# Kernel optimization log

Measured on AMD Instinct MI355X. Metric: run time of the kernel, lower is better.

Reference implementation:

```python
import jax, jax.numpy as jnp
import numpy as np

D_MODEL = 1024
D_STATE = 16
D_CONV = 4
EXPAND = 2
D_INNER = D_MODEL * EXPAND


def setup_inputs() -> dict:
    key = jax.random.key(0)
    ks = jax.random.split(key, 8)
    B, L = 2, 2048
    x = jax.random.normal(ks[0], (B, L, D_MODEL), dtype=jnp.float32)
    # in_proj: Linear(d_model -> 2*d_inner), no bias
    W_in = jax.random.normal(ks[1], (D_MODEL, 2 * D_INNER), dtype=jnp.float32) / np.sqrt(D_MODEL)
    # depthwise conv1d: (d_inner, 1, d_conv) + bias
    conv_w = jax.random.normal(ks[2], (D_INNER, 1, D_CONV), dtype=jnp.float32) / np.sqrt(D_CONV)
    conv_b = jax.random.normal(ks[3], (D_INNER,), dtype=jnp.float32) * 0.01
    # x_proj: Linear(d_inner -> 2*d_state + 1), no bias
    W_x = jax.random.normal(ks[4], (D_INNER, 2 * D_STATE + 1), dtype=jnp.float32) / np.sqrt(D_INNER)
    # A_log ~ Uniform(-log(d_state), -1)
    A_log = jax.random.uniform(ks[5], (D_INNER, D_STATE), dtype=jnp.float32,
                               minval=-np.log(D_STATE), maxval=-1.0)
    D_param = jnp.ones((D_INNER,), dtype=jnp.float32)
    W_out = jax.random.normal(ks[6], (D_INNER, D_MODEL), dtype=jnp.float32) / np.sqrt(D_INNER)
    return {"x": x, "W_in": W_in, "conv_w": conv_w, "conv_b": conv_b,
            "W_x": W_x, "A_log": A_log, "D_param": D_param, "W_out": W_out}


def _selective_scan(x, delta, A, Bm, Cm):
    # x:(B,L,D), delta:(B,L), A:(D,N), Bm/Cm:(B,L,N)
    Bsz, L, Dd = x.shape
    N = A.shape[1]
    h0 = jnp.zeros((Bsz, Dd, N), dtype=x.dtype)

    def step(h, inp):
        dt, Bt, Ct, xt = inp  # (B,), wait dt:(B,), Bt:(B,N), Ct:(B,N), xt:(B,D)
        A_bar = jnp.exp(dt[:, None, None] * A)          # (B,D,N)
        dB = (dt[:, None] * Bt)[:, None, :]             # (B,1,N)
        h = A_bar * h + dB * xt[:, :, None]             # (B,D,N)
        y = jnp.einsum('bn,bdn->bd', Ct, h)             # (B,D)
        return h, y

    xs = (jnp.swapaxes(delta, 0, 1), jnp.swapaxes(Bm, 0, 1),
          jnp.swapaxes(Cm, 0, 1), jnp.swapaxes(x, 0, 1))
    _, ys = jax.lax.scan(step, h0, xs)                  # ys: (L,B,D)
    return jnp.swapaxes(ys, 0, 1)


def reference(x, W_in, conv_w, conv_b, W_x, A_log, D_param, W_out):
    B, L, _ = x.shape
    xr = x @ W_in                                       # (B,L,2*Di)
    x_inner, res = jnp.split(xr, 2, axis=-1)
    # causal depthwise conv: left-pad d_conv-1, valid conv == torch slice [:L]
    xc = jnp.swapaxes(x_inner, 1, 2)                    # (B,Di,L)
    xc = jax.lax.conv_general_dilated(
        xc, conv_w, window_strides=(1,), padding=[(D_CONV - 1, 0)],
        dimension_numbers=('NCH', 'OIH', 'NCH'), feature_group_count=D_INNER)
    xc = xc + conv_b[None, :, None]
    xc = jnp.swapaxes(xc, 1, 2)                         # (B,L,Di)
    xc = jax.nn.silu(xc)
    ssm_params = xc @ W_x                               # (B,L,1+2N)
    delta = jax.nn.softplus(ssm_params[..., 0])         # (B,L)
    Bm = ssm_params[..., 1:1 + D_STATE]                 # (B,L,N)
    Cm = ssm_params[..., 1 + D_STATE:]                  # (B,L,N)
    A = -jnp.exp(A_log)                                 # (Di,N)
    y = _selective_scan(xc, delta, A, Bm, Cm)           # (B,L,Di)
    y = y + xc * D_param[None, None, :]
    y = y * jax.nn.silu(res)
    return y @ W_out                                    # (B,L,d_model)
```

## Files before the change

kernel.cpp:

```cpp
#include <hip/hip_runtime.h>

#define L_SEQ 2048
#define NB    2
#define DMOD  1024
#define DIN   2048
#define NST   16
#define NROWS (NB*L_SEQ)
#define CL    64
#define NC    (L_SEQ/CL)

typedef unsigned short u16;
typedef _Float16 half8 __attribute__((ext_vector_type(8)));
typedef float f32x4 __attribute__((ext_vector_type(4)));
typedef short short8 __attribute__((ext_vector_type(8)));

__device__ __forceinline__ float siluf(float v){ return v / (1.f + __expf(-v)); }
__device__ __forceinline__ u16 f2h_bits(float v){ _Float16 h = (_Float16)v; return __builtin_bit_cast(u16, h); }
__device__ __forceinline__ float h2f(u16 v){ return (float)__builtin_bit_cast(_Float16, v); }
__device__ __forceinline__ float fexp2(float x){
#if __has_builtin(__builtin_amdgcn_exp2f)
    return __builtin_amdgcn_exp2f(x);
#else
    return __expf(x * 0.69314718056f);
#endif
}

__device__ __forceinline__ void gload16(const u16* g, u16* l)
{
    __builtin_amdgcn_global_load_lds(
        (const __attribute__((address_space(1))) void*)g,
        (__attribute__((address_space(3))) void*)l,
        16, 0, 0);
}

#define BARRIER() do { asm volatile("" ::: "memory"); __builtin_amdgcn_s_barrier(); asm volatile("" ::: "memory"); } while (0)
#define VMCNT0()  asm volatile("s_waitcnt vmcnt(0)" ::: "memory")
#define VMCNT2()  asm volatile("s_waitcnt vmcnt(2)" ::: "memory")
#define VMCNT4()  asm volatile("s_waitcnt vmcnt(4)" ::: "memory")
#define VMCNT8()  asm volatile("s_waitcnt vmcnt(8)" ::: "memory")

__global__ __launch_bounds__(256)
void prep_inputs(const float* __restrict__ x, const float* __restrict__ W_in,
                 const float* __restrict__ W_out, const float* __restrict__ Wx,
                 u16* __restrict__ x16, u16* __restrict__ Bt1,
                 u16* __restrict__ Bt3, u16* __restrict__ WxT16)
{
    __shared__ float s[64][65];
    const int bid = blockIdx.x, tid = threadIdx.x;
    if (bid < 4096) {
        int i = bid * 256 + tid;
        float4 v = ((const float4*)x)[i];
        ushort4 o;
        o.x = f2h_bits(v.x); o.y = f2h_bits(v.y); o.z = f2h_bits(v.z); o.w = f2h_bits(v.w);
        *(ushort4*)&x16[(size_t)i * 4] = o;
    } else if (bid < 5632) {
        const float* in; u16* outT; int R, C, rblk, cblk;
        if (bid < 5120) { int b = bid - 4096; in = W_in;  outT = Bt1; R = 1024; C = 4096; cblk = b & 63; rblk = b >> 6; }
        else            { int b = bid - 5120; in = W_out; outT = Bt3; R = 2048; C = 1024; cblk = b & 15; rblk = b >> 4; }
        int r0 = rblk * 64, c0 = cblk * 64;
        int tc = tid & 63, ty = tid >> 6;
        #pragma unroll
        for (int j = 0; j < 16; j++) {
            int r = ty + j * 4;
            s[r][tc] = in[(size_t)(r0 + r) * C + c0 + tc];
        }
        __syncthreads();
        #pragma unroll
        for (int j = 0; j < 16; j++) {
            int nn = ty + j * 4;
            outT[(size_t)(c0 + nn) * R + r0 + tc] = f2h_bits(s[tc][nn]);
        }
    } else {
        int idx = (bid - 5632) * 256 + tid;
        int n = idx >> 11, k = idx & 2047;
        float v = (n < 33) ? Wx[k * 33 + n] : 0.f;
        WxT16[idx] = f2h_bits(v);
    }
}

template<int EPI>
__global__ __launch_bounds__(512, 2)
void gemm8b(const u16* __restrict__ A, const u16* __restrict__ Bt,
            void* __restrict__ C0v, void* __restrict__ C1v,
            int M, int N, int KLEN, int lda, int ldb)
{
    __shared__ __align__(16) u16 As[2 * 256 * 64];
    __shared__ __align__(16) u16 Bs[2 * 256 * 64];
    const int tid  = threadIdx.x;
    const int lane = tid & 63;
    const int w    = tid >> 6;
    const int wm   = w >> 2, wn = w & 3;
    const int bm = blockIdx.y * 256, bn = blockIdx.x * 256;
    const int kBase = blockIdx.z * KLEN;

    const int srow8 = lane >> 3;
    const int sunit = (lane & 7) ^ srow8;
    const u16* Ag = A  + (size_t)(bm + srow8) * lda + kBase + sunit * 8;
    const u16* Bg = Bt + (size_t)(bn + srow8) * ldb + kBase + sunit * 8;
    const int rw = w * 16;

    const int fr  = lane & 15;
    const int sl0 = ((lane >> 4) ^ (fr & 7)) * 8;
    int aOffs[8], bOffs[4];
    #pragma unroll
    for (int mi = 0; mi < 8; mi++) aOffs[mi] = (wm * 128 + mi * 16 + fr) * 64 + sl0;
    #pragma unroll
    for (int ni = 0; ni < 4; ni++) bOffs[ni] = (ni * 64 + wn * 16 + fr) * 64 + sl0;

    f32x4 acc[8][4];
    #pragma unroll
    for (int i = 0; i < 8; i++)
        #pragma unroll
        for (int j = 0; j < 4; j++)
            acc[i][j] = (f32x4){0.f, 0.f, 0.f, 0.f};

    auto stage2 = [&](const u16* G, int ld, int rbase, int kcol, u16* ldsDst) {
        gload16(G + (size_t)rbase * ld + kcol, ldsDst);
        gload16(G + (size_t)(rbase + 8) * ld + kcol, ldsDst + 8 * 64);
    };

    const int NT = KLEN >> 6;
    stage2(Ag, lda, 0 + rw, 0, &As[(0 + rw) * 64]);
    stage2(Ag, lda, 128 + rw, 0, &As[(128 + rw) * 64]);
    stage2(Bg, ldb, 0 + rw, 0, &Bs[(0 + rw) * 64]);
    stage2(Bg, ldb, 128 + rw, 0, &Bs[(128 + rw) * 64]);

    for (int t = 0; t < NT; ++t) {
        const int cO = (t & 1) << 14;
        const int nO = cO ^ 16384;
        const int kn = (t + 1) << 6;
        const bool pf = (t + 1) < NT;

        VMCNT2();
        BARRIER();

        half8 a0[8], a1[8];
        #pragma unroll
        for (int mi = 0; mi < 8; mi++) {
            a0[mi] = *(const half8*)&As[cO + aOffs[mi]];
            a1[mi] = *(const half8*)&As[cO + (aOffs[mi] ^ 32)];
        }
        half8 b00 = *(const half8*)&Bs[cO + bOffs[0]];
        half8 b01 = *(const half8*)&Bs[cO + (bOffs[0] ^ 32)];
        half8 b10 = *(const half8*)&Bs[cO + bOffs[1]];
        half8 b11 = *(const half8*)&Bs[cO + (bOffs[1] ^ 32)];
        if (pf) {
            stage2(Ag, lda, 0 + rw, kn, &As[nO + (0 + rw) * 64]);
            stage2(Ag, lda, 128 + rw, kn, &As[nO + (128 + rw) * 64]);
        }
        #pragma unroll
        for (int mi = 0; mi < 8; mi++) {
            acc[mi][0] = __builtin_amdgcn_mfma_f32_16x16x32_f16(a0[mi], b00, acc[mi][0], 0, 0, 0);
            acc[mi][0] = __builtin_amdgcn_mfma_f32_16x16x32_f16(a1[mi], b01, acc[mi][0], 0, 0, 0);
        }
        #pragma unroll
        for (int mi = 0; mi < 8; mi++) {
            acc[mi][1] = __builtin_amdgcn_mfma_f32_16x16x32_f16(a0[mi], b10, acc[mi][1], 0, 0, 0);
            acc[mi][1] = __builtin_amdgcn_mfma_f32_16x16x32_f16(a1[mi], b11, acc[mi][1], 0, 0, 0);
        }
        if (pf) VMCNT4(); else VMCNT0();
        BARRIER();

        b00 = *(const half8*)&Bs[cO + bOffs[2]];
        b01 = *(const half8*)&Bs[cO + (bOffs[2] ^ 32)];
        b10 = *(const half8*)&Bs[cO + bOffs[3]];
        b11 = *(const half8*)&Bs[cO + (bOffs[3] ^ 32)];
        if (pf) {
            stage2(Bg, ldb, 0 + rw, kn, &Bs[nO + (0 + rw) * 64]);
            stage2(Bg, ldb, 128 + rw, kn, &Bs[nO + (128 + rw) * 64]);
        }
        #pragma unroll
        for (int mi = 0; mi < 8; mi++) {
            acc[mi][2] = __builtin_amdgcn_mfma_f32_16x16x32_f16(a0[mi], b00, acc[mi][2], 0, 0, 0);
            acc[mi][2] = __builtin_amdgcn_mfma_f32_16x16x32_f16(a1[mi], b01, acc[mi][2], 0, 0, 0);
        }
        #pragma unroll
        for (int mi = 0; mi < 8; mi++) {
            acc[mi][3] = __builtin_amdgcn_mfma_f32_16x16x32_f16(a0[mi], b10, acc[mi][3], 0, 0, 0);
            acc[mi][3] = __builtin_amdgcn_mfma_f32_16x16x32_f16(a1[mi], b11, acc[mi][3], 0, 0, 0);
        }
    }

    const int cr = (lane >> 4) * 4;
    #pragma unroll
    for (int mi = 0; mi < 8; mi++) {
        #pragma unroll
        for (int ni = 0; ni < 4; ni++) {
            #pragma unroll
            for (int q = 0; q < 4; q++) {
                int row = bm + wm * 128 + mi * 16 + cr + q;
                int col = bn + ni * 64 + wn * 16 + fr;
                float v = acc[mi][ni][q];
                int half = N >> 1;
                if (col < half) ((u16*)C0v)[(size_t)row * half + col] = f2h_bits(v);
                else            ((u16*)C1v)[(size_t)row * half + col - half] = f2h_bits(siluf(v));
            }
        }
    }
}

__global__ __launch_bounds__(256, 2)
void gemm128c(const u16* __restrict__ A, const u16* __restrict__ Bt,
              u16* __restrict__ C0, int M, int N, int KLEN, int lda, int ldb)
{
    __shared__ __align__(16) u16 As[2 * 128 * 64];
    __shared__ __align__(16) u16 Bs[2 * 128 * 64];
    const int tid  = threadIdx.x;
    const int lane = tid & 63;
    const int wid  = tid >> 6;
    const int wm   = wid >> 1, wn = wid & 1;
    const int bm = blockIdx.y * 128, bn = blockIdx.x * 128;
    const int kBase = blockIdx.z * KLEN;

    const int srow8 = lane >> 3;
    const int sunit = (lane & 7) ^ srow8;
    const u16* Ag = A  + (size_t)(bm + srow8) * lda + kBase + sunit * 8;
    const u16* Bg = Bt + (size_t)(bn + srow8) * ldb + kBase + sunit * 8;

    const int fr = lane & 15;
    const int s0 = ((lane >> 4) ^ (lane & 7)) * 8;
    const int aBase = (wm * 64 + fr) * 64 + s0;
    const int bBase = (wn * 64 + fr) * 64 + s0;

    f32x4 acc[4][4];
    #pragma unroll
    for (int i = 0; i < 4; i++)
        #pragma unroll
        for (int j = 0; j < 4; j++)
            acc[i][j] = (f32x4){0.f, 0.f, 0.f, 0.f};

    auto STAGE = [&](int bufO, int k0) {
        #pragma unroll
        for (int j = 0; j < 4; j++) {
            int c = wid * 4 + j;
            gload16(Ag + (size_t)(c * 8) * lda + k0, &As[bufO + c * 512]);
            gload16(Bg + (size_t)(c * 8) * ldb + k0, &Bs[bufO + c * 512]);
        }
    };

    auto COMPUTE = [&](int bufO) {
        #pragma unroll
        for (int kk = 0; kk < 2; kk++) {
            const int x = kk ? 32 : 0;
            half8 af[4], bf[4];
            #pragma unroll
            for (int mi = 0; mi < 4; mi++)
                af[mi] = *(const half8*)&As[bufO + (aBase ^ x) + mi * 1024];
            #pragma unroll
            for (int ni = 0; ni < 4; ni++)
                bf[ni] = *(const half8*)&Bs[bufO + (bBase ^ x) + ni * 1024];
            #pragma unroll
            for (int mi = 0; mi < 4; mi++)
                #pragma unroll
                for (int ni = 0; ni < 4; ni++)
                    acc[mi][ni] = __builtin_amdgcn_mfma_f32_16x16x32_f16(af[mi], bf[ni], acc[mi][ni], 0, 0, 0);
        }
    };

    const int NT = KLEN >> 6;
    STAGE(0, 0);
    int buf = 0;
    for (int t = 0; t < NT; ++t) {
        if (t + 1 < NT) { STAGE(buf ^ 8192, (t + 1) << 6); VMCNT8(); }
        else            { VMCNT0(); }
        BARRIER();
        COMPUTE(buf);
        BARRIER();
        buf ^= 8192;
    }

    const int cr = (lane >> 4) * 4;
    const int cc = lane & 15;
    #pragma unroll
    for (int mi = 0; mi < 4; mi++) {
        #pragma unroll
        for (int ni = 0; ni < 4; ni++) {
            #pragma unroll
            for (int q = 0; q < 4; q++) {
                int row = bm + wm * 64 + mi * 16 + cr + q;
                int col = bn + wn * 64 + ni * 16 + cc;
                C0[((size_t)blockIdx.z * M + row) * N + col] = f2h_bits(acc[mi][ni][q]);
            }
        }
    }
}

__global__ __launch_bounds__(256)
void add_partials(const u16* __restrict__ p, float* __restrict__ out)
{
    int i = blockIdx.x * 256 + threadIdx.x;
    short8 a = *(const short8*)&p[(size_t)i * 8];
    short8 b = *(const short8*)&p[(size_t)NROWS * DMOD + (size_t)i * 8];
    float4 o0, o1;
    o0.x = h2f((u16)a[0]) + h2f((u16)b[0]);
    o0.y = h2f((u16)a[1]) + h2f((u16)b[1]);
    o0.z = h2f((u16)a[2]) + h2f((u16)b[2]);
    o0.w = h2f((u16)a[3]) + h2f((u16)b[3]);
    o1.x = h2f((u16)a[4]) + h2f((u16)b[4]);
    o1.y = h2f((u16)a[5]) + h2f((u16)b[5]);
    o1.z = h2f((u16)a[6]) + h2f((u16)b[6]);
    o1.w = h2f((u16)a[7]) + h2f((u16)b[7]);
    *(float4*)&out[(size_t)i * 8]     = o0;
    *(float4*)&out[(size_t)i * 8 + 4] = o1;
}

__global__ __launch_bounds__(256)
void conv_silu16t(const u16* __restrict__ xin16, const float* __restrict__ cw,
                  const float* __restrict__ cb, u16* __restrict__ xc16)
{
    __shared__ u16 sx[35][136];
    const int d0 = blockIdx.x << 7, t0 = blockIdx.y << 5, b = blockIdx.z;
    const int tid = threadIdx.x;
    for (int i = tid; i < 35 * 16; i += 256) {
        int r = i >> 4, u = i & 15;
        int t = t0 - 3 + r;
        short8 v = {0,0,0,0,0,0,0,0};
        if (t >= 0) v = *(const short8*)&xin16[((size_t)(b * L_SEQ + t)) * DIN + d0 + u * 8];
        *(short8*)&sx[r][u * 8] = v;
    }
    __syncthreads();
    const int u  = tid & 15;
    const int tl = tid >> 4;
    const int d  = d0 + u * 8;
    const float4* cw4 = (const float4*)cw;
    float4 w[8];
    #pragma unroll
    for (int j = 0; j < 8; j++) w[j] = cw4[d + j];
    float bias[8];
    {
        float4 b0 = *(const float4*)&cb[d];
        float4 b1 = *(const float4*)&cb[d + 4];
        bias[0]=b0.x; bias[1]=b0.y; bias[2]=b0.z; bias[3]=b0.w;
        bias[4]=b1.x; bias[5]=b1.y; bias[6]=b1.z; bias[7]=b1.w;
    }
    #pragma unroll
    for (int half = 0; half < 2; half++) {
        const int t_l = tl + half * 16;
        float acc[8];
        #pragma unroll
        for (int j = 0; j < 8; j++) acc[j] = bias[j];
        #pragma unroll
        for (int k = 0; k < 4; k++) {
            short8 v = *(const short8*)&sx[t_l + k][u * 8];
            #pragma unroll
            for (int j = 0; j < 8; j++)
                acc[j] = fmaf(h2f((u16)v[j]), (&w[j].x)[k], acc[j]);
        }
        short8 o;
        #pragma unroll
        for (int j = 0; j < 8; j++) o[j] = (short)f2h_bits(siluf(acc[j]));
        *(short8*)&xc16[((size_t)(b * L_SEQ + t0 + t_l)) * DIN + d] = o;
    }
}

__global__ __launch_bounds__(256)
void gemm2_mfma(const u16* __restrict__ A, const u16* __restrict__ Bt, float* __restrict__ pb)
{
    __shared__ __align__(16) u16 As[64 * 64];
    __shared__ __align__(16) u16 Bs[48 * 64];
    const int tid = threadIdx.x, lane = tid & 63, w = tid >> 6;
    const int bm = blockIdx.x * 64;
    const int kz = blockIdx.y;
    const int arow = tid >> 2;
    const int au   = (tid & 3) << 1;
    f32x4 acc[3];
    acc[0] = acc[1] = acc[2] = (f32x4){0.f, 0.f, 0.f, 0.f};

    for (int it = 0; it < 4; ++it) {
        const int k0 = kz * 256 + it * 64;
        short8 ra0 = *(const short8*)&A[(size_t)(bm + arow) * DIN + k0 + au * 8];
        short8 ra1 = *(const short8*)&A[(size_t)(bm + arow) * DIN + k0 + (au + 1) * 8];
        short8 rb0, rb1;
        if (tid < 192) {
            rb0 = *(const short8*)&Bt[(size_t)arow * DIN + k0 + au * 8];
            rb1 = *(const short8*)&Bt[(size_t)arow * DIN + k0 + (au + 1) * 8];
        }
        __syncthreads();
        {
            int s0 = au ^ (arow & 7), s1 = (au + 1) ^ (arow & 7);
            *(short8*)&As[arow * 64 + s0 * 8] = ra0;
            *(short8*)&As[arow * 64 + s1 * 8] = ra1;
            if (tid < 192) {
                *(short8*)&Bs[arow * 64 + s0 * 8] = rb0;
                *(short8*)&Bs[arow * 64 + s1 * 8] = rb1;
            }
        }
        __syncthreads();
        #pragma unroll
        for (int kk = 0; kk < 2; kk++) {
            int r = w * 16 + (lane & 15);
            int sl = (kk * 4 + (lane >> 4)) ^ (r & 7);
            half8 af = *(const half8*)&As[r * 64 + sl * 8];
            #pragma unroll
            for (int ni = 0; ni < 3; ni++) {
                int br = ni * 16 + (lane & 15);
                int bsl = (kk * 4 + (lane >> 4)) ^ (br & 7);
                half8 bf = *(const half8*)&Bs[br * 64 + bsl * 8];
                acc[ni] = __builtin_amdgcn_mfma_f32_16x16x32_f16(af, bf, acc[ni], 0, 0, 0);
            }
        }
    }
    #pragma unroll
    for (int ni = 0; ni < 3; ni++) {
        #pragma unroll
        for (int q = 0; q < 4; q++) {
            int row = bm + w * 16 + (lane >> 4) * 4 + q;
            int col = ni * 16 + (lane & 15);
            pb[((size_t)kz * NROWS + row) * 48 + col] = acc[ni][q];
        }
    }
}

__global__ __launch_bounds__(256)
void gemm2_reduce(const float* __restrict__ pb, float* __restrict__ delta,
                  float* __restrict__ Bm, float* __restrict__ Cm)
{
    int idx = blockIdx.x * 256 + threadIdx.x;
    int row = idx / 48, col = idx - row * 48;
    float s = 0.f;
    #pragma unroll
    for (int kz = 0; kz < 8; kz++) s += pb[(size_t)kz * NROWS * 48 + idx];
    if (col == 0)       delta[row] = fmaxf(s, 0.f) + log1pf(__expf(-fabsf(s)));
    else if (col < 17)  Bm[row * NST + col - 1]  = s;
    else if (col < 33)  Cm[row * NST + col - 17] = s;
}

__global__ __launch_bounds__(256)
void scan_part1_reg(const u16* __restrict__ xc16, const float* __restrict__ delta,
                    const float* __restrict__ Bm, const float* __restrict__ A_log,
                    u16* __restrict__ h16, float* __restrict__ Sc)
{
    const int b = blockIdx.z, c = blockIdx.y;
    const int d = blockIdx.x * 256 + threadIdx.x;
    float ka[16];
    {
        const float4* Av = (const float4*)(A_log + (size_t)d * 16);
        #pragma unroll
        for (int q = 0; q < 4; q++) {
            float4 a = Av[q];
            ka[q*4+0] = -__expf(a.x) * 1.44269504f;
            ka[q*4+1] = -__expf(a.y) * 1.44269504f;
            ka[q*4+2] = -__expf(a.z) * 1.44269504f;
            ka[q*4+3] = -__expf(a.w) * 1.44269504f;
        }
    }
    float h[16];
    #pragma unroll
    for (int n = 0; n < 16; n++) h[n] = 0.f;
    float S = 0.f;
    const int rowbase = b * L_SEQ + c * CL;
    #pragma unroll 2
    for (int t = 0; t < CL; ++t) {
        const int rowg = rowbase + t;
        const float dt = delta[rowg];
        const float4* Bv = (const float4*)(Bm + (size_t)rowg * 16);
        float4 b0 = Bv[0], b1 = Bv[1], b2 = Bv[2], b3 = Bv[3];
        float bb[16] = {b0.x,b0.y,b0.z,b0.w, b1.x,b1.y,b1.z,b1.w,
                        b2.x,b2.y,b2.z,b2.w, b3.x,b3.y,b3.z,b3.w};
        const float xt = h2f(xc16[(size_t)rowg * DIN + d]);
        const float dtx = dt * xt;
        S += dt;
        #pragma unroll
        for (int n = 0; n < 16; n++) {
            float a = fexp2(dt * ka[n]);
            h[n] = fmaf(a, h[n], bb[n] * dtx);
        }
    }
    u16* hp = h16 + (((size_t)(b * NC + c) * DIN) + d) * 16;
    short8 o0, o1;
    #pragma unroll
    for (int j = 0; j < 8; j++) { o0[j] = (short)f2h_bits(h[j]); o1[j] = (short)f2h_bits(h[8 + j]); }
    *(short8*)&hp[0] = o0;
    *(short8*)&hp[8] = o1;
    if (threadIdx.x == 0 && blockIdx.x == 0) Sc[b * NC + c] = S;
}

__global__ __launch_bounds__(256)
void scan_carry(const u16* __restrict__ h16, const float* __restrict__ Sc,
                const float* __restrict__ A_log, u16* __restrict__ H16)
{
    int gid = blockIdx.x * 256 + threadIdx.x;
    int b = gid >> 15, r = gid & 32767;
    const float ka = -__expf(A_log[r]) * 1.44269504f;
    float H = 0.f;
    for (int c = 0; c < NC; ++c) {
        size_t idx = ((size_t)(b * NC + c) << 15) + r;
        H16[idx] = f2h_bits(H);
        float P = fexp2(Sc[b * NC + c] * ka);
        H = fmaf(P, H, h2f(h16[idx]));
    }
}

__global__ __launch_bounds__(256)
void scan_part3_reg(const u16* __restrict__ xc16, const float* __restrict__ delta,
                    const float* __restrict__ Bm, const float* __restrict__ Cm,
                    const float* __restrict__ A_log, const float* __restrict__ Dp,
                    const u16* __restrict__ res16, const u16* __restrict__ H16,
                    u16* __restrict__ yh)
{
    const int b = blockIdx.z, c = blockIdx.y;
    const int d = blockIdx.x * 256 + threadIdx.x;
    float ka[16];
    {
        const float4* Av = (const float4*)(A_log + (size_t)d * 16);
        #pragma unroll
        for (int q = 0; q < 4; q++) {
            float4 a = Av[q];
            ka[q*4+0] = -__expf(a.x) * 1.44269504f;
            ka[q*4+1] = -__expf(a.y) * 1.44269504f;
            ka[q*4+2] = -__expf(a.z) * 1.44269504f;
            ka[q*4+3] = -__expf(a.w) * 1.44269504f;
        }
    }
    float h[16];
    {
        const u16* Hp = H16 + (((size_t)(b * NC + c) * DIN) + d) * 16;
        short8 v0 = *(const short8*)&Hp[0];
        short8 v1 = *(const short8*)&Hp[8];
        #pragma unroll
        for (int j = 0; j < 8; j++) { h[j] = h2f((u16)v0[j]); h[8 + j] = h2f((u16)v1[j]); }
    }
    const float Dpd = Dp[d];
    const int rowbase = b * L_SEQ + c * CL;
    #pragma unroll 2
    for (int t = 0; t < CL; ++t) {
        const int rowg = rowbase + t;
        const float dt = delta[rowg];
        const float4* Bv = (const float4*)(Bm + (size_t)rowg * 16);
        const float4* Cv = (const float4*)(Cm + (size_t)rowg * 16);
        float4 b0 = Bv[0], b1 = Bv[1], b2 = Bv[2], b3 = Bv[3];
        float4 c0 = Cv[0], c1 = Cv[1], c2 = Cv[2], c3 = Cv[3];
        float bb[16] = {b0.x,b0.y,b0.z,b0.w, b1.x,b1.y,b1.z,b1.w,
                        b2.x,b2.y,b2.z,b2.w, b3.x,b3.y,b3.z,b3.w};
        float cc[16] = {c0.x,c0.y,c0.z,c0.w, c1.x,c1.y,c1.z,c1.w,
                        c2.x,c2.y,c2.z,c2.w, c3.x,c3.y,c3.z,c3.w};
        const float xt = h2f(xc16[(size_t)rowg * DIN + d]);
        const float rt = h2f(res16[(size_t)rowg * DIN + d]);
        const float dtx = dt * xt;
        float y = 0.f;
        #pragma unroll
        for (int n = 0; n < 16; n++) {
            float a = fexp2(dt * ka[n]);
            h[n] = fmaf(a, h[n], bb[n] * dtx);
            y = fmaf(cc[n], h[n], y);
        }
        y = (y + xt * Dpd) * rt;
        yh[(size_t)rowg * DIN + d] = f2h_bits(y);
    }
}

extern "C" void kernel_launch(void* const* d_in, const int* in_sizes, int n_in,
                              void* d_out, int out_size, void* d_ws, size_t ws_size,
                              hipStream_t stream)
{
    const float* x     = (const float*)d_in[0];
    const float* W_in  = (const float*)d_in[1];
    const float* cw    = (const float*)d_in[2];
    const float* cb    = (const float*)d_in[3];
    const float* Wx    = (const float*)d_in[4];
    const float* A_log = (const float*)d_in[5];
    const float* Dp    = (const float*)d_in[6];
    const float* W_out = (const float*)d_in[7];
    float* out = (float*)d_out;
    float* ws  = (float*)d_ws;

    u16*   xin16 = (u16*)(ws);
    u16*   y16   = (u16*)(ws);
    u16*   res16 = (u16*)(ws + 4194304);
    u16*   xc16  = (u16*)(ws + 8388608);
    u16*   x16   = (u16*)(ws + 12582912);
    u16*   p2    = (u16*)(ws + 12582912);
    u16*   Bt1   = (u16*)(ws + 14680064);
    float* pb    = ws + 14680064;
    u16*   WxT16 = (u16*)(ws + 20971520);
    float* delta = ws + 21020672;
    float* Bm    = ws + 21024768;
    float* Cm    = ws + 21090304;
    float* Sc    = ws + 21155840;
    u16*   h16   = (u16*)(ws + 21156864);
    u16*   H16   = (u16*)(ws + 22205440);
    u16*   Bt3   = (u16*)(ws + 23254016);

    dim3 blk(256), blk512(512);

    prep_inputs<<<dim3(6016), blk, 0, stream>>>(x, W_in, W_out, Wx, x16, Bt1, Bt3, WxT16);
    gemm8b<1><<<dim3(16, 16, 1), blk512, 0, stream>>>(x16, Bt1, xin16, res16,
                                                      NROWS, 2 * DIN, DMOD, DMOD, DMOD);
    conv_silu16t<<<dim3(DIN / 128, L_SEQ / 32, NB), blk, 0, stream>>>(xin16, cw, cb, xc16);
    gemm2_mfma<<<dim3(NROWS / 64, 8), blk, 0, stream>>>(xc16, WxT16, pb);
    gemm2_reduce<<<dim3(NROWS * 48 / 256), blk, 0, stream>>>(pb, delta, Bm, Cm);
    scan_part1_reg<<<dim3(DIN / 256, NC, NB), blk, 0, stream>>>(xc16, delta, Bm, A_log, h16, Sc);
    scan_carry<<<dim3(NB * DIN * NST / 256), blk, 0, stream>>>(h16, Sc, A_log, H16);
    scan_part3_reg<<<dim3(DIN / 256, NC, NB), blk, 0, stream>>>(xc16, delta, Bm, Cm, A_log, Dp, res16, H16, y16);
    gemm128c<<<dim3(DMOD / 128, NROWS / 128, 2), blk, 0, stream>>>(y16, Bt3, p2,
                                                                   NROWS, DMOD, DIN / 2, DIN, DIN);
    add_partials<<<dim3(NROWS * DMOD / 8 / 256), blk, 0, stream>>>(p2, out);
}
```

Before: 178.7 us.

## Fuse x_proj GEMM split-K reduction into single kernel with in-block LDS reduce

Replaces the split-K x_proj GEMM, which wrote fp32 partials to global memory and needed a separate reduce kernel, with one kernel. Each block handles 16 rows, and its four waves split K four ways. MFMA operands are loaded straight from global memory with no LDS staging, and the wave partials are summed in shared memory before softplus and the B/C writes. This removes a kernel launch and the global partial-buffer round trip. The cost is fewer blocks (256) and uncoalesced global fragment loads, with the 48-row weight matrix reread by every block.

```diff
diff --git a/kernel.cpp b/kernel.cpp
--- a/kernel.cpp
+++ b/kernel.cpp
@@ -354,75 +354,45 @@
 }
 
 __global__ __launch_bounds__(256)
-void gemm2_mfma(const u16* __restrict__ A, const u16* __restrict__ Bt, float* __restrict__ pb)
-{
-    __shared__ __align__(16) u16 As[64 * 64];
-    __shared__ __align__(16) u16 Bs[48 * 64];
+void gemm2s(const u16* __restrict__ A, const u16* __restrict__ Bt,
+            float* __restrict__ delta, float* __restrict__ Bm, float* __restrict__ Cm)
+{
+    __shared__ float sred[4][16][48];
     const int tid = threadIdx.x, lane = tid & 63, w = tid >> 6;
-    const int bm = blockIdx.x * 64;
-    const int kz = blockIdx.y;
-    const int arow = tid >> 2;
-    const int au   = (tid & 3) << 1;
+    const int bm = blockIdx.x * 16;
+    const int fr = lane & 15;
+    const int ko = (lane >> 4) * 8;
     f32x4 acc[3];
     acc[0] = acc[1] = acc[2] = (f32x4){0.f, 0.f, 0.f, 0.f};
-
-    for (int it = 0; it < 4; ++it) {
-        const int k0 = kz * 256 + it * 64;
-        short8 ra0 = *(const short8*)&A[(size_t)(bm + arow) * DIN + k0 + au * 8];
-        short8 ra1 = *(const short8*)&A[(size_t)(bm + arow) * DIN + k0 + (au + 1) * 8];
-        short8 rb0, rb1;
-        if (tid < 192) {
-            rb0 = *(const short8*)&Bt[(size_t)arow * DIN + k0 + au * 8];
-            rb1 = *(const short8*)&Bt[(size_t)arow * DIN + k0 + (au + 1) * 8];
-        }
-        __syncthreads();
-        {
-            int s0 = au ^ (arow & 7), s1 = (au + 1) ^ (arow & 7);
-            *(short8*)&As[arow * 64 + s0 * 8] = ra0;
-            *(short8*)&As[arow * 64 + s1 * 8] = ra1;
-            if (tid < 192) {
-                *(short8*)&Bs[arow * 64 + s0 * 8] = rb0;
-                *(short8*)&Bs[arow * 64 + s1 * 8] = rb1;
-            }
-        }
-        __syncthreads();
+    const int kw = w * 512;
+    #pragma unroll
+    for (int t = 0; t < 8; ++t) {
+        const int k0 = kw + t * 64;
         #pragma unroll
         for (int kk = 0; kk < 2; kk++) {
-            int r = w * 16 + (lane & 15);
-            int sl = (kk * 4 + (lane >> 4)) ^ (r & 7);
-            half8 af = *(const half8*)&As[r * 64 + sl * 8];
+            const int kc = k0 + kk * 32 + ko;
+            half8 af = *(const half8*)&A[(size_t)(bm + fr) * DIN + kc];
             #pragma unroll
             for (int ni = 0; ni < 3; ni++) {
-                int br = ni * 16 + (lane & 15);
-                int bsl = (kk * 4 + (lane >> 4)) ^ (br & 7);
-                half8 bf = *(const half8*)&Bs[br * 64 + bsl * 8];
+                half8 bf = *(const half8*)&Bt[(size_t)(ni * 16 + fr) * DIN + kc];
                 acc[ni] = __builtin_amdgcn_mfma_f32_16x16x32_f16(af, bf, acc[ni], 0, 0, 0);
             }
         }
     }
     #pragma unroll
-    for (int ni = 0; ni < 3; ni++) {
-        #pragma unroll
-        for (int q = 0; q < 4; q++) {
-            int row = bm + w * 16 + (lane >> 4) * 4 + q;
-            int col = ni * 16 + (lane & 15);
-            pb[((size_t)kz * NROWS + row) * 48 + col] = acc[ni][q];
-        }
-    }
-}
-
-__global__ __launch_bounds__(256)
-void gemm2_reduce(const float* __restrict__ pb, float* __restrict__ delta,
-                  float* __restrict__ Bm, float* __restrict__ Cm)
-{
-    int idx = blockIdx.x * 256 + threadIdx.x;
-    int row = idx / 48, col = idx - row * 48;
-    float s = 0.f;
-    #pragma unroll
-    for (int kz = 0; kz < 8; kz++) s += pb[(size_t)kz * NROWS * 48 + idx];
-    if (col == 0)       delta[row] = fmaxf(s, 0.f) + log1pf(__expf(-fabsf(s)));
-    else if (col < 17)  Bm[row * NST + col - 1]  = s;
-    else if (col < 33)  Cm[row * NST + col - 17] = s;
+    for (int ni = 0; ni < 3; ni++)
+        #pragma unroll
+        for (int q = 0; q < 4; q++)
+            sred[w][(lane >> 4) * 4 + q][ni * 16 + fr] = acc[ni][q];
+    __syncthreads();
+    for (int i = tid; i < 16 * 48; i += 256) {
+        int r = i / 48, c = i - r * 48;
+        float s = sred[0][r][c] + sred[1][r][c] + sred[2][r][c] + sred[3][r][c];
+        int row = bm + r;
+        if (c == 0)      delta[row] = fmaxf(s, 0.f) + log1pf(__expf(-fabsf(s)));
+        else if (c < 17) Bm[row * NST + c - 1]  = s;
+        else if (c < 33) Cm[row * NST + c - 17] = s;
+    }
 }
 
 __global__ __launch_bounds__(256)
@@ -571,7 +541,6 @@
     u16*   x16   = (u16*)(ws + 12582912);
     u16*   p2    = (u16*)(ws + 12582912);
     u16*   Bt1   = (u16*)(ws + 14680064);
-    float* pb    = ws + 14680064;
     u16*   WxT16 = (u16*)(ws + 20971520);
     float* delta = ws + 21020672;
     float* Bm    = ws + 21024768;
@@ -587,8 +556,7 @@
     gemm8b<1><<<dim3(16, 16, 1), blk512, 0, stream>>>(x16, Bt1, xin16, res16,
                                                       NROWS, 2 * DIN, DMOD, DMOD, DMOD);
     conv_silu16t<<<dim3(DIN / 128, L_SEQ / 32, NB), blk, 0, stream>>>(xin16, cw, cb, xc16);
-    gemm2_mfma<<<dim3(NROWS / 64, 8), blk, 0, stream>>>(xc16, WxT16, pb);
-    gemm2_reduce<<<dim3(NROWS * 48 / 256), blk, 0, stream>>>(pb, delta, Bm, Cm);
+    gemm2s<<<dim3(NROWS / 16), blk, 0, stream>>>(xc16, WxT16, delta, Bm, Cm);
     scan_part1_reg<<<dim3(DIN / 256, NC, NB), blk, 0, stream>>>(xc16, delta, Bm, A_log, h16, Sc);
     scan_carry<<<dim3(NB * DIN * NST / 256), blk, 0, stream>>>(h16, Sc, A_log, H16);
     scan_part3_reg<<<dim3(DIN / 256, NC, NB), blk, 0, stream>>>(xc16, delta, Bm, Cm, A_log, Dp, res16, H16, y16);
```

Result: no change. 179.3 us (+0.3%).
